# Kernel tuning notes

Measured on AMD Instinct MI355X. Metric: run time of the kernel, lower is better.

The kernel has to match this reference:

```python
import jax, jax.numpy as jnp
import numpy as np

N_NODES = 100000
K_NBRS = 16
N_EDGES = N_NODES * K_NBRS


def setup_inputs() -> dict:
    key = jax.random.key(0)
    ks = jax.random.split(key, 20)
    x = jax.random.normal(ks[0], (N_NODES, 3), dtype=jnp.float32)
    # knn-like edge list: every node is the target of exactly K_NBRS edges
    dst = jnp.repeat(jnp.arange(N_NODES, dtype=jnp.int64), K_NBRS)
    src = jax.random.randint(ks[1], (N_EDGES,), 0, N_NODES, dtype=jnp.int64)
    edge_index = jnp.stack([src, dst], axis=0)  # [2, E], row0=source(j), row1=target(i)

    def lin_init(k, fan_in, fan_out):
        s = 1.0 / np.sqrt(fan_in)
        return jax.random.uniform(k, (fan_in, fan_out), jnp.float32, -s, s)

    inp = {"x": x, "edge_index": edge_index}
    inp["W1"], inp["b1"] = lin_init(ks[2], 6, 64), jnp.zeros((64,), jnp.float32)
    for i, kk in zip(range(2, 6), ks[3:7]):
        inp[f"W{i}"] = lin_init(kk, 128, 64)
        inp[f"b{i}"] = jnp.zeros((64,), jnp.float32)
    inp["Wa"], inp["ba"] = lin_init(ks[8], 128, 128), jnp.zeros((128,), jnp.float32)
    inp["Wb"], inp["bb"] = lin_init(ks[9], 128, 3), jnp.zeros((3,), jnp.float32)
    return inp


def edge_conv(x, src, dst, W, b):
    # PyG EdgeConv: message = nn(cat([x_i, x_j - x_i])), max-aggregate at target i
    xi = x[dst]                      # [E, C] center (target) features
    xj = x[src]                      # [E, C] neighbor (source) features
    msg = jnp.concatenate([xi, xj - xi], axis=-1)  # [E, 2C]
    msg = jax.nn.relu(msg @ W + b)                 # [E, 64] per-edge MLP
    return jax.ops.segment_max(msg, dst, num_segments=N_NODES)  # [N, 64]


def reference(x, edge_index, W1, b1, W2, b2, W3, b3, W4, b4, W5, b5, Wa, ba, Wb, bb):
    src, dst = edge_index[0], edge_index[1]
    h = edge_conv(x, src, dst, W1, b1)
    h = edge_conv(h, src, dst, W2, b2)
    h = edge_conv(h, src, dst, W3, b3)
    h = edge_conv(h, src, dst, W4, b4)
    h = edge_conv(h, src, dst, W5, b5)           # [N, 64]
    g = jnp.max(h, axis=0, keepdims=True)        # [1, 64] global max
    feat = jnp.concatenate([h, jnp.broadcast_to(g, h.shape)], axis=1)  # [N, 128]
    out = jax.nn.relu(feat @ Wa + ba) @ Wb + bb  # [N, 3]
    return x + out
```

## Files before the change

kernel.cpp:

```cpp
#include <hip/hip_runtime.h>
#include <math.h>

#define N_NODES 100000
#define K_NBRS 16
#define N_EDGES (N_NODES * K_NBRS)
#define TPB 256
#define NBLK 2048

typedef __attribute__((ext_vector_type(8))) short short8;
typedef __attribute__((ext_vector_type(4))) float float4_;
typedef __attribute__((ext_vector_type(4))) int int4_;
typedef __attribute__((ext_vector_type(4))) unsigned short ushort4_;

__device__ __forceinline__ unsigned short f2bf(float f) {
  unsigned int u = __float_as_uint(f);
  u += 0x7fffu + ((u >> 16) & 1u);
  return (unsigned short)(u >> 16);
}
__device__ __forceinline__ float bf2f(unsigned short b) {
  return __uint_as_float(((unsigned int)b) << 16);
}

__global__ void k_pre(const int* __restrict__ ei, int* __restrict__ srcout,
                      const float* __restrict__ x, const float* __restrict__ W1,
                      const float* __restrict__ b1,
                      unsigned short* __restrict__ A, unsigned short* __restrict__ B) {
  const bool is64 = (ei[1] == 0) && (ei[3] == 0) && (ei[5] == 0) && (ei[7] == 0);
  const int tid = blockIdx.x * blockDim.x + threadIdx.x;
  const int stride = gridDim.x * blockDim.x;
  for (int e = tid; e < N_EDGES; e += stride)
    srcout[e] = is64 ? ei[2 * e] : ei[e];

  const int lane = threadIdx.x & 63;
  const int nwaves = stride >> 6;
  const int wid0 = tid >> 6;
  float w[6];
#pragma unroll
  for (int k = 0; k < 6; ++k) w[k] = W1[k * 64 + lane];
  const float bias = b1[lane];
  for (int i0 = wid0; i0 < N_NODES; i0 += nwaves) {
    const int i = __builtin_amdgcn_readfirstlane(i0);
    const float x0 = x[3 * i], x1 = x[3 * i + 1], x2 = x[3 * i + 2];
    const float b = fmaf(x0, w[3], fmaf(x1, w[4], x2 * w[5]));
    const float a = bias + fmaf(x0, w[0] - w[3],
                          fmaf(x1, w[1] - w[4], x2 * (w[2] - w[5])));
    A[(size_t)i * 64 + lane] = f2bf(a);
    B[(size_t)i * 64 + lane] = f2bf(b);
  }
}

template <bool DO_GMAX>
__global__ void k_aggr(const int* __restrict__ src,
                       const unsigned short* __restrict__ Ain,
                       const unsigned short* __restrict__ Bin,
                       unsigned short* __restrict__ hout, float* __restrict__ P) {
  const int lane = threadIdx.x & 63;
  const int q = lane >> 4;
  const int c4 = (lane & 15) * 4;
  const int nw = (gridDim.x * blockDim.x) >> 6;
  const int w0 = (blockIdx.x * blockDim.x + threadIdx.x) >> 6;
  float4_ gmax = (float4_)(0.f);
  int p = w0;
  int4_ idx[4];
  ushort4_ avp;
  if (p * 4 < N_NODES) {
    const int i0 = __builtin_amdgcn_readfirstlane(p * 4);
#pragma unroll
    for (int n = 0; n < 4; ++n)
      idx[n] = *(const int4_*)(src + (size_t)(i0 + n) * 16 + q * 4);
    avp = *(const ushort4_*)(Ain + (size_t)(i0 + q) * 64 + c4);
  }
  while (p * 4 < N_NODES) {
    const int i0 = __builtin_amdgcn_readfirstlane(p * 4);
    ushort4_ gv[4][4];
#pragma unroll
    for (int n = 0; n < 4; ++n)
#pragma unroll
      for (int e = 0; e < 4; ++e)
        gv[n][e] = *(const ushort4_*)(Bin + (size_t)idx[n][e] * 64 + c4);
    const int pn = p + nw;
    int4_ idxn[4];
    ushort4_ avn;
    if (pn * 4 < N_NODES) {
      const int i1 = __builtin_amdgcn_readfirstlane(pn * 4);
#pragma unroll
      for (int n = 0; n < 4; ++n)
        idxn[n] = *(const int4_*)(src + (size_t)(i1 + n) * 16 + q * 4);
      avn = *(const ushort4_*)(Ain + (size_t)(i1 + q) * 64 + c4);
    }
    float4_ m[4];
#pragma unroll
    for (int n = 0; n < 4; ++n) {
#pragma unroll
      for (int t = 0; t < 4; ++t) {
        const float v0 = bf2f(gv[n][0][t]), v1 = bf2f(gv[n][1][t]);
        const float v2 = bf2f(gv[n][2][t]), v3 = bf2f(gv[n][3][t]);
        m[n][t] = fmaxf(fmaxf(v0, v1), fmaxf(v2, v3));
      }
#pragma unroll
      for (int t = 0; t < 4; ++t) {
        float v = m[n][t];
        v = fmaxf(v, __shfl_xor(v, 16));
        v = fmaxf(v, __shfl_xor(v, 32));
        m[n][t] = v;
      }
    }
    ushort4_ hb;
#pragma unroll
    for (int t = 0; t < 4; ++t) {
      float v = m[0][t];
      v = (q == 1) ? m[1][t] : v;
      v = (q == 2) ? m[2][t] : v;
      v = (q == 3) ? m[3][t] : v;
      const float h = fmaxf(bf2f(avp[t]) + v, 0.f);
      hb[t] = f2bf(h);
      if constexpr (DO_GMAX) gmax[t] = fmaxf(gmax[t], h);
    }
    *(ushort4_*)(hout + (size_t)(i0 + q) * 64 + c4) = hb;
    p = pn;
#pragma unroll
    for (int n = 0; n < 4; ++n) idx[n] = idxn[n];
    avp = avn;
  }
  if constexpr (DO_GMAX) {
    __shared__ float red[TPB][4];
#pragma unroll
    for (int t = 0; t < 4; ++t) red[threadIdx.x][t] = gmax[t];
    __syncthreads();
    if (threadIdx.x < 64) {
      const int c = threadIdx.x, j = c >> 2, t = c & 3;
      float mm = 0.f;
#pragma unroll
      for (int w = 0; w < 4; ++w)
#pragma unroll
        for (int qq = 0; qq < 4; ++qq)
          mm = fmaxf(mm, red[w * 64 + qq * 16 + j][t]);
      P[(size_t)blockIdx.x * 64 + c] = mm;
    }
  }
}

__global__ __launch_bounds__(TPB, 2)
void k_gemm(const unsigned short* __restrict__ h, const float* __restrict__ W,
            const float* __restrict__ bn,
            unsigned short* __restrict__ Aout, unsigned short* __restrict__ Bout) {
  __shared__ unsigned short lwhi[128 * 72];
  __shared__ unsigned short lwlo[128 * 72];
  for (int idx = threadIdx.x; idx < 8192; idx += TPB) {
    const int k = idx >> 7, j = idx & 127;
    const float v = (j < 64) ? (W[k * 64 + j] - W[(64 + k) * 64 + j])
                             : W[(64 + k) * 64 + (j - 64)];
    const unsigned short hi = f2bf(v);
    lwhi[j * 72 + k] = hi;
    lwlo[j * 72 + k] = f2bf(v - bf2f(hi));
  }
  __syncthreads();
  const int lane = threadIdx.x & 63;
  const int wav = threadIdx.x >> 6;
  const int l15 = lane & 15, lg = lane >> 4;
  short8 bhi[8][2], blo[8][2];
#pragma unroll
  for (int ct = 0; ct < 8; ++ct)
#pragma unroll
    for (int kk = 0; kk < 2; ++kk) {
      const int off = (ct * 16 + l15) * 72 + kk * 32 + lg * 8;
      bhi[ct][kk] = *(const short8*)&lwhi[off];
      blo[ct][kk] = *(const short8*)&lwlo[off];
    }
  float bv[4];
#pragma unroll
  for (int ct = 0; ct < 4; ++ct) bv[ct] = bn[ct * 16 + l15];
  const int NT = (N_NODES + 63) / 64;
  for (int t = blockIdx.x; t < NT; t += gridDim.x) {
    const int nb = t * 64 + wav * 16;
    const int row = min(nb + l15, N_NODES - 1);
    const unsigned short* hr = h + (size_t)row * 64;
    float4_ acc[8];
#pragma unroll
    for (int ct = 0; ct < 8; ++ct) acc[ct] = (float4_)(0.f);
#pragma unroll
    for (int kk = 0; kk < 2; ++kk) {
      const short8 ahi = *(const short8*)(hr + kk * 32 + lg * 8);
#pragma unroll
      for (int ct = 0; ct < 8; ++ct) {
        acc[ct] = __builtin_amdgcn_mfma_f32_16x16x32_bf16(ahi, bhi[ct][kk], acc[ct], 0, 0, 0);
        acc[ct] = __builtin_amdgcn_mfma_f32_16x16x32_bf16(ahi, blo[ct][kk], acc[ct], 0, 0, 0);
      }
    }
#pragma unroll
    for (int ct = 0; ct < 8; ++ct)
#pragma unroll
      for (int r = 0; r < 4; ++r) {
        const int node = nb + lg * 4 + r;
        if (node < N_NODES) {
          if (ct < 4)
            Aout[(size_t)node * 64 + ct * 16 + l15] = f2bf(acc[ct][r] + bv[ct]);
          else
            Bout[(size_t)node * 64 + (ct - 4) * 16 + l15] = f2bf(acc[ct][r]);
        }
      }
  }
}

__global__ void k_gred(const float* __restrict__ P, float* __restrict__ g) {
  __shared__ float red[16][64];
  const int lane = threadIdx.x & 63;
  const int w = threadIdx.x >> 6;
  float m = 0.f;
  for (int r = w; r < NBLK; r += 16)
    m = fmaxf(m, P[(size_t)r * 64 + lane]);
  red[w][lane] = m;
  __syncthreads();
  if (threadIdx.x < 64) {
    float mm = 0.f;
#pragma unroll
    for (int k = 0; k < 16; ++k) mm = fmaxf(mm, red[k][lane]);
    g[lane] = mm;
  }
}

__global__ __launch_bounds__(TPB, 2)
void k_final(const unsigned short* __restrict__ h, const float* __restrict__ g,
             const float* __restrict__ Wa, const float* __restrict__ ba,
             const float* __restrict__ Wb, const float* __restrict__ bb,
             const float* __restrict__ x, float* __restrict__ out) {
  __shared__ unsigned short lwhi[128 * 72];
  __shared__ unsigned short lwlo[128 * 72];
  __shared__ float sgt[128];
  for (int idx = threadIdx.x; idx < 8192; idx += TPB) {
    const int k = idx >> 7, j = idx & 127;
    const float v = Wa[k * 128 + j];
    const unsigned short hi = f2bf(v);
    lwhi[j * 72 + k] = hi;
    lwlo[j * 72 + k] = f2bf(v - bf2f(hi));
  }
  if (threadIdx.x < 128) {
    const int c = threadIdx.x;
    float s = ba[c];
    for (int k = 0; k < 64; ++k) s = fmaf(g[k], Wa[(64 + k) * 128 + c], s);
    sgt[c] = s;
  }
  __syncthreads();
  const int lane = threadIdx.x & 63;
  const int wav = threadIdx.x >> 6;
  const int l15 = lane & 15, lg = lane >> 4;
  short8 bhi[8][2], blo[8][2];
#pragma unroll
  for (int ct = 0; ct < 8; ++ct)
#pragma unroll
    for (int kk = 0; kk < 2; ++kk) {
      const int off = (ct * 16 + l15) * 72 + kk * 32 + lg * 8;
      bhi[ct][kk] = *(const short8*)&lwhi[off];
      blo[ct][kk] = *(const short8*)&lwlo[off];
    }
  float gtv[8];
#pragma unroll
  for (int ct = 0; ct < 8; ++ct) gtv[ct] = sgt[ct * 16 + l15];
  float wbv[8][3];
#pragma unroll
  for (int ct = 0; ct < 8; ++ct)
#pragma unroll
    for (int jj = 0; jj < 3; ++jj)
      wbv[ct][jj] = Wb[(ct * 16 + l15) * 3 + jj];
  const float bbl = (l15 == 0) ? bb[0] : (l15 == 1 ? bb[1] : bb[2]);
  const int NT = (N_NODES + 63) / 64;
  for (int t = blockIdx.x; t < NT; t += gridDim.x) {
    const int nb = t * 64 + wav * 16;
    const int row = min(nb + l15, N_NODES - 1);
    const unsigned short* hr = h + (size_t)row * 64;
    float4_ acc[8];
#pragma unroll
    for (int ct = 0; ct < 8; ++ct) acc[ct] = (float4_)(0.f);
#pragma unroll
    for (int kk = 0; kk < 2; ++kk) {
      const short8 ahi = *(const short8*)(hr + kk * 32 + lg * 8);
#pragma unroll
      for (int ct = 0; ct < 8; ++ct) {
        acc[ct] = __builtin_amdgcn_mfma_f32_16x16x32_bf16(ahi, bhi[ct][kk], acc[ct], 0, 0, 0);
        acc[ct] = __builtin_amdgcn_mfma_f32_16x16x32_bf16(ahi, blo[ct][kk], acc[ct], 0, 0, 0);
      }
    }
#pragma unroll
    for (int r = 0; r < 4; ++r) {
      float t0 = 0.f, t1 = 0.f, t2 = 0.f;
#pragma unroll
      for (int ct = 0; ct < 8; ++ct) {
        const float hd = fmaxf(acc[ct][r] + gtv[ct], 0.f);
        t0 = fmaf(hd, wbv[ct][0], t0);
        t1 = fmaf(hd, wbv[ct][1], t1);
        t2 = fmaf(hd, wbv[ct][2], t2);
      }
#pragma unroll
      for (int off = 1; off < 16; off <<= 1) {
        t0 += __shfl_xor(t0, off);
        t1 += __shfl_xor(t1, off);
        t2 += __shfl_xor(t2, off);
      }
      const int node = nb + lg * 4 + r;
      if (node < N_NODES && l15 < 3) {
        const float tj = (l15 == 0) ? t0 : (l15 == 1 ? t1 : t2);
        out[(size_t)node * 3 + l15] = x[(size_t)node * 3 + l15] + tj + bbl;
      }
    }
  }
}

extern "C" void kernel_launch(void* const* d_in, const int* in_sizes, int n_in,
                              void* d_out, int out_size, void* d_ws, size_t ws_size,
                              hipStream_t stream) {
  const float* x  = (const float*)d_in[0];
  const int*   ei = (const int*)d_in[1];
  const float* W1 = (const float*)d_in[2];
  const float* b1 = (const float*)d_in[3];
  const float* W2 = (const float*)d_in[4];
  const float* b2 = (const float*)d_in[5];
  const float* W3 = (const float*)d_in[6];
  const float* b3 = (const float*)d_in[7];
  const float* W4 = (const float*)d_in[8];
  const float* b4 = (const float*)d_in[9];
  const float* W5 = (const float*)d_in[10];
  const float* b5 = (const float*)d_in[11];
  const float* Wa = (const float*)d_in[12];
  const float* ba = (const float*)d_in[13];
  const float* Wb = (const float*)d_in[14];
  const float* bb = (const float*)d_in[15];
  float* out = (float*)d_out;

  float* ws = (float*)d_ws;
  int* srcbuf = (int*)ws;
  unsigned short* A0 = (unsigned short*)(ws + 1600000);
  unsigned short* A1 = A0 + 6400000;
  unsigned short* H  = A1 + 6400000;
  unsigned short* B0 = H + 6400000;
  unsigned short* B1 = B0 + 6400000;
  float* P = (float*)(B1 + 6400000);
  float* g = P + (size_t)NBLK * 64;

  k_pre<<<NBLK, TPB, 0, stream>>>(ei, srcbuf, x, W1, b1, A0, B0);
  k_aggr<false><<<NBLK, TPB, 0, stream>>>(srcbuf, A0, B0, H, nullptr);
  k_gemm<<<1024, TPB, 0, stream>>>(H, W2, b2, A1, B1);
  k_aggr<false><<<NBLK, TPB, 0, stream>>>(srcbuf, A1, B1, H, nullptr);
  k_gemm<<<1024, TPB, 0, stream>>>(H, W3, b3, A0, B0);
  k_aggr<false><<<NBLK, TPB, 0, stream>>>(srcbuf, A0, B0, H, nullptr);
  k_gemm<<<1024, TPB, 0, stream>>>(H, W4, b4, A1, B1);
  k_aggr<false><<<NBLK, TPB, 0, stream>>>(srcbuf, A1, B1, H, nullptr);
  k_gemm<<<1024, TPB, 0, stream>>>(H, W5, b5, A0, B0);
  k_aggr<true><<<NBLK, TPB, 0, stream>>>(srcbuf, A0, B0, H, P);
  k_gred<<<1, 1024, 0, stream>>>(P, g);
  k_final<<<1024, TPB, 0, stream>>>(H, g, Wa, ba, Wb, bb, x, out);
}
```

Before: 400.2 us.

## Simplify aggregation to per-quarter-wave node gather, drop software prefetch

The aggregation kernel now has each 16-lane group handle one node's 16 neighbors directly. This replaces the cross-group shuffle reduction and the software-pipelined prefetch of the next node's indices. It removes the shuffles and the select chain, but gives up explicit prefetch overlap and reads indices per group instead of coalesced across groups. The change also aligns the LDS weight arrays to 16 bytes, reorders the workspace buffers, and halves the final kernel's grid.

```diff
diff --git a/kernel.cpp b/kernel.cpp
--- a/kernel.cpp
+++ b/kernel.cpp
@@ -60,67 +60,38 @@
   const int nw = (gridDim.x * blockDim.x) >> 6;
   const int w0 = (blockIdx.x * blockDim.x + threadIdx.x) >> 6;
   float4_ gmax = (float4_)(0.f);
-  int p = w0;
-  int4_ idx[4];
-  ushort4_ avp;
-  if (p * 4 < N_NODES) {
-    const int i0 = __builtin_amdgcn_readfirstlane(p * 4);
-#pragma unroll
-    for (int n = 0; n < 4; ++n)
-      idx[n] = *(const int4_*)(src + (size_t)(i0 + n) * 16 + q * 4);
-    avp = *(const ushort4_*)(Ain + (size_t)(i0 + q) * 64 + c4);
-  }
-  while (p * 4 < N_NODES) {
-    const int i0 = __builtin_amdgcn_readfirstlane(p * 4);
-    ushort4_ gv[4][4];
-#pragma unroll
-    for (int n = 0; n < 4; ++n)
+  for (int p = w0; p * 4 < N_NODES; p += nw) {
+    const int i = __builtin_amdgcn_readfirstlane(p * 4) + q;
+    const int* sp = src + (size_t)i * K_NBRS;
+    int4_ idx[4];
+#pragma unroll
+    for (int e4 = 0; e4 < 4; ++e4)
+      idx[e4] = *(const int4_*)(sp + e4 * 4);
+    ushort4_ gv[16];
+#pragma unroll
+    for (int e4 = 0; e4 < 4; ++e4)
 #pragma unroll
       for (int e = 0; e < 4; ++e)
-        gv[n][e] = *(const ushort4_*)(Bin + (size_t)idx[n][e] * 64 + c4);
-    const int pn = p + nw;
-    int4_ idxn[4];
-    ushort4_ avn;
-    if (pn * 4 < N_NODES) {
-      const int i1 = __builtin_amdgcn_readfirstlane(pn * 4);
-#pragma unroll
-      for (int n = 0; n < 4; ++n)
-        idxn[n] = *(const int4_*)(src + (size_t)(i1 + n) * 16 + q * 4);
-      avn = *(const ushort4_*)(Ain + (size_t)(i1 + q) * 64 + c4);
-    }
-    float4_ m[4];
-#pragma unroll
-    for (int n = 0; n < 4; ++n) {
-#pragma unroll
-      for (int t = 0; t < 4; ++t) {
-        const float v0 = bf2f(gv[n][0][t]), v1 = bf2f(gv[n][1][t]);
-        const float v2 = bf2f(gv[n][2][t]), v3 = bf2f(gv[n][3][t]);
-        m[n][t] = fmaxf(fmaxf(v0, v1), fmaxf(v2, v3));
-      }
-#pragma unroll
-      for (int t = 0; t < 4; ++t) {
-        float v = m[n][t];
-        v = fmaxf(v, __shfl_xor(v, 16));
-        v = fmaxf(v, __shfl_xor(v, 32));
-        m[n][t] = v;
-      }
-    }
+        gv[e4 * 4 + e] = *(const ushort4_*)(Bin + (size_t)idx[e4][e] * 64 + c4);
+    const ushort4_ av = *(const ushort4_*)(Ain + (size_t)i * 64 + c4);
     ushort4_ hb;
 #pragma unroll
     for (int t = 0; t < 4; ++t) {
-      float v = m[0][t];
-      v = (q == 1) ? m[1][t] : v;
-      v = (q == 2) ? m[2][t] : v;
-      v = (q == 3) ? m[3][t] : v;
-      const float h = fmaxf(bf2f(avp[t]) + v, 0.f);
+      float m01 = fmaxf(bf2f(gv[0][t]), bf2f(gv[1][t]));
+      float m23 = fmaxf(bf2f(gv[2][t]), bf2f(gv[3][t]));
+      float m45 = fmaxf(bf2f(gv[4][t]), bf2f(gv[5][t]));
+      float m67 = fmaxf(bf2f(gv[6][t]), bf2f(gv[7][t]));
+      float m89 = fmaxf(bf2f(gv[8][t]), bf2f(gv[9][t]));
+      float mab = fmaxf(bf2f(gv[10][t]), bf2f(gv[11][t]));
+      float mcd = fmaxf(bf2f(gv[12][t]), bf2f(gv[13][t]));
+      float mef = fmaxf(bf2f(gv[14][t]), bf2f(gv[15][t]));
+      const float m = fmaxf(fmaxf(fmaxf(m01, m23), fmaxf(m45, m67)),
+                            fmaxf(fmaxf(m89, mab), fmaxf(mcd, mef)));
+      const float h = fmaxf(bf2f(av[t]) + m, 0.f);
       hb[t] = f2bf(h);
       if constexpr (DO_GMAX) gmax[t] = fmaxf(gmax[t], h);
     }
-    *(ushort4_*)(hout + (size_t)(i0 + q) * 64 + c4) = hb;
-    p = pn;
-#pragma unroll
-    for (int n = 0; n < 4; ++n) idx[n] = idxn[n];
-    avp = avn;
+    *(ushort4_*)(hout + (size_t)i * 64 + c4) = hb;
   }
   if constexpr (DO_GMAX) {
     __shared__ float red[TPB][4];
@@ -144,8 +115,8 @@
 void k_gemm(const unsigned short* __restrict__ h, const float* __restrict__ W,
             const float* __restrict__ bn,
             unsigned short* __restrict__ Aout, unsigned short* __restrict__ Bout) {
-  __shared__ unsigned short lwhi[128 * 72];
-  __shared__ unsigned short lwlo[128 * 72];
+  __shared__ __align__(16) unsigned short lwhi[128 * 72];
+  __shared__ __align__(16) unsigned short lwlo[128 * 72];
   for (int idx = threadIdx.x; idx < 8192; idx += TPB) {
     const int k = idx >> 7, j = idx & 127;
     const float v = (j < 64) ? (W[k * 64 + j] - W[(64 + k) * 64 + j])
@@ -224,8 +195,8 @@
              const float* __restrict__ Wa, const float* __restrict__ ba,
              const float* __restrict__ Wb, const float* __restrict__ bb,
              const float* __restrict__ x, float* __restrict__ out) {
-  __shared__ unsigned short lwhi[128 * 72];
-  __shared__ unsigned short lwlo[128 * 72];
+  __shared__ __align__(16) unsigned short lwhi[128 * 72];
+  __shared__ __align__(16) unsigned short lwlo[128 * 72];
   __shared__ float sgt[128];
   for (int idx = threadIdx.x; idx < 8192; idx += TPB) {
     const int k = idx >> 7, j = idx & 127;
@@ -329,11 +300,11 @@
   float* ws = (float*)d_ws;
   int* srcbuf = (int*)ws;
   unsigned short* A0 = (unsigned short*)(ws + 1600000);
-  unsigned short* A1 = A0 + 6400000;
-  unsigned short* H  = A1 + 6400000;
-  unsigned short* B0 = H + 6400000;
-  unsigned short* B1 = B0 + 6400000;
-  float* P = (float*)(B1 + 6400000);
+  unsigned short* B0 = A0 + 6400000;
+  unsigned short* A1 = B0 + 6400000;
+  unsigned short* B1 = A1 + 6400000;
+  unsigned short* H  = B1 + 6400000;
+  float* P = (float*)(H + 6400000);
   float* g = P + (size_t)NBLK * 64;
 
   k_pre<<<NBLK, TPB, 0, stream>>>(ei, srcbuf, x, W1, b1, A0, B0);
@@ -347,5 +318,5 @@
   k_gemm<<<1024, TPB, 0, stream>>>(H, W5, b5, A0, B0);
   k_aggr<true><<<NBLK, TPB, 0, stream>>>(srcbuf, A0, B0, H, P);
   k_gred<<<1, 1024, 0, stream>>>(P, g);
-  k_final<<<1024, TPB, 0, stream>>>(H, g, Wa, ba, Wb, bb, x, out);
-}
+  k_final<<<512, TPB, 0, stream>>>(H, g, Wa, ba, Wb, bb, x, out);
+}
```

Result: faster. 384.7 us (-3.9%).
